# Kernel optimization log

Hardware: AMD Instinct MI355X
Metric: run time of the kernel (lower is better)

The kernel has to match this reference:

```python
import jax, jax.numpy as jnp
import numpy as np

IGNORE = 255
KA = 10.0
ITERS = 10
BETA = 0.8


def _l2(x, axis):
    # F.normalize(p=2): divide by max(norm, eps)
    return x / jnp.maximum(jnp.linalg.norm(x, axis=axis, keepdims=True), 1e-12)


def setup_inputs() -> dict:
    key = jax.random.key(0)
    k1, k2, k3, k4 = jax.random.split(key, 4)
    B, K, P, C = 8, 19, 16384, 256
    return {
        "logit": jax.random.normal(k1, (B, K, P), jnp.float32),
        "target": jax.random.randint(k2, (B, P), 0, K, jnp.int32),
        "feat": jax.random.normal(k3, (B, C, P), jnp.float32),
        "epoch": 60,
        "prototypes_dataset": _l2(jax.random.normal(k4, (C, K), jnp.float32), 0),
    }


def reference(logit, target, feat, epoch, prototypes_dataset):
    B, K, P = logit.shape
    C = feat.shape[1]
    dt = feat.dtype

    # scatter-sum per-class prototypes over all (b, p) positions; ignore bucket = K
    index = jnp.where(target == IGNORE, K, target).reshape(-1)            # [B*P]
    feat_flat = jnp.swapaxes(feat, 1, 2).reshape(B * P, C)                # [B*P, C]
    proto = jax.ops.segment_sum(feat_flat, index, num_segments=K + 1)    # [K+1, C]
    counts = jax.ops.segment_sum(jnp.ones_like(index), index, num_segments=K + 1)
    prototypes_sum = proto[:K].T                                          # [C, K]
    counts_batch = counts[:K]                                             # [K]

    # epoch is a static python int; epoch >= start_epoch(51) -> full vMF branch
    feat_norm = _l2(feat, 1)                                              # [B, C, P]
    u_init = _l2(prototypes_sum / (counts_batch.astype(dt) + 1e-6), 0)    # [C, K]
    mask0 = counts_batch == 0
    u = _l2(jnp.where(mask0[None, :], prototypes_dataset, u_init), 0)     # 'part' init
    a = jnp.full((1, 1, K), 1.0 / K, dt)

    dis = jnp.einsum('bcp,ck->bpk', feat_norm, u)                         # [B, P, K]
    e = a * jnp.exp(KA * dis)
    p = e / jnp.sum(e, -1, keepdims=True)
    for _ in range(ITERS):
        # 'avmf': second assignment in torch overwrites -> mean over batch, [1, P, K]
        a = jnp.mean(p, 0, keepdims=True)
        # 'uvmf': new prototypes from soft assignments
        u = _l2(jnp.mean(jnp.einsum('bcp,bpk->bck', feat_norm, p), 0), 0)
        dis = jnp.einsum('bcp,ck->bpk', feat_norm, u)
        e = a * jnp.exp(KA * dis)
        p = e / jnp.sum(e, -1, keepdims=True)

    # vMF_hard_loss computed in torch but 'hard' not in loss_type -> not added
    vmf_loss = jnp.mean(-p * (jnp.log(a + 1e-6) + KA * dis)) / float(np.log(K))
    consist_loss = jnp.mean(-jnp.swapaxes(p, 1, 2) * jax.nn.log_softmax(logit, axis=1))

    # contrast: off-diagonal prototype similarity over classes present in batch
    m = (~mask0).astype(dt)
    gram = u_init.T @ u_init                                              # [K, K]
    Kn = jnp.sum(m)
    contrast_loss = (jnp.sum(gram * (m[:, None] * m[None, :])) - Kn) / (Kn * (Kn - 1))

    # 'tce': truncated CE, clamp per-pixel loss at -log(beta)
    logp = jax.nn.log_softmax(logit, axis=1)                              # [B, K, P]
    safe_t = jnp.where(target == IGNORE, 0, target)
    ce = -jnp.take_along_axis(logp, safe_t[:, None, :], axis=1)[:, 0, :]  # [B, P]
    valid = (target != IGNORE).astype(dt)
    loss = jnp.sum(jnp.maximum(ce, -float(np.log(BETA))) * valid) / (jnp.sum(valid) + 1e-6)

    loss = loss + vmf_loss + contrast_loss + consist_loss
    return (loss, jax.lax.stop_gradient(prototypes_sum), jax.lax.stop_gradient(counts_batch))
```

## Files before the change

kernel.cpp:

```cpp
#include <hip/hip_runtime.h>
#include <hip/hip_bf16.h>
#include <math.h>

#define BB 8
#define KK 19
#define PP 16384
#define CC 256
#define NN (BB*PP)
#define KA_C 10.0f
#define IGNORE_L 255
#define CETHR 0.22314355131420976f
#define AQ 524288

#define OFF_FEATN   0
#define OFF_FEATNT  16777216
#define OFF_PROTO   33554432
#define OFF_COUNTS  (OFF_PROTO+4864)
#define OFF_SCAL    (OFF_COUNTS+32)
#define OFF_UINIT   (OFF_SCAL+16)
#define OFF_U       (OFF_UINIT+4864)
#define OFF_UBF     (OFF_U+4864)
#define OFF_A       (OFF_UBF+4224)
#define OFF_UPART   (OFF_A+8*AQ)
#define OFF_R1      (OFF_UPART+4980736)
#define OFF_NORM    (OFF_R1+77824)

typedef __attribute__((ext_vector_type(8))) short short8v;
typedef __attribute__((ext_vector_type(4))) float f32x4;

static __device__ __forceinline__ float bflo(unsigned int v){
    union{unsigned int i; float f;} x; x.i = v << 16; return x.f;
}
static __device__ __forceinline__ unsigned short f2bf(float f){
    union{float f; unsigned int i;} x; x.f = f;
    unsigned int r = (x.i + 0x7fffu + ((x.i >> 16) & 1u)) >> 16;
    return (unsigned short)r;
}
static __device__ __forceinline__ float rowsum16(float v){
    v += __shfl_xor(v,1); v += __shfl_xor(v,2);
    v += __shfl_xor(v,4); v += __shfl_xor(v,8);
    return v;
}

__global__ __launch_bounds__(256) void counts_kernel(const int* __restrict__ target,
                                                     float* __restrict__ ws) {
    __shared__ int cnt[KK];
    if (threadIdx.x < KK) cnt[threadIdx.x]=0;
    __syncthreads();
    for (int i = blockIdx.x*256 + threadIdx.x; i < NN; i += gridDim.x*256) {
        int t = target[i];
        if (t >= 0 && t < KK) atomicAdd(&cnt[t], 1);
    }
    __syncthreads();
    if (threadIdx.x < KK) atomicAdd(&ws[OFF_COUNTS + threadIdx.x], (float)cnt[threadIdx.x]);
}

__global__ __launch_bounds__(256) void ssct_kernel(const float* __restrict__ feat,
                                                   unsigned short* __restrict__ featn,
                                                   unsigned short* __restrict__ featn_T,
                                                   float* __restrict__ normf) {
    __shared__ float part[4][64];
    __shared__ float rn_lds[64];
    __shared__ unsigned short tTus[64][270];
    int blk = blockIdx.x;
    int b = blk >> 8;
    int px0 = (blk & 255) * 64;
    int tid = threadIdx.x;
    int l = tid & 63, w = tid >> 6;
    const float* fb = feat + (size_t)b*CC*PP;
    int c0 = w*64;
    float ss = 0.f;
    for (int cc=0; cc<64; cc++) {
        float v = fb[(size_t)(c0+cc)*PP + px0 + l];
        ss = fmaf(v, v, ss);
    }
    part[w][l] = ss;
    __syncthreads();
    if (tid < 64) {
        float s = part[0][tid]+part[1][tid]+part[2][tid]+part[3][tid];
        float nrm = fmaxf(sqrtf(s), 1e-12f);
        normf[(size_t)b*PP + px0 + tid] = nrm;
        rn_lds[tid] = 1.0f/nrm;
    }
    __syncthreads();
    float r = rn_lds[l];
    unsigned short* ob  = featn + (size_t)b*CC*PP + px0;
    for (int cc=0; cc<64; cc++) {
        int c = c0 + cc;
        float v = fb[(size_t)c*PP + px0 + l];
        unsigned short us = f2bf(v * r);
        ob[(size_t)c*PP + l] = us;
        tTus[l][c] = us;
    }
    __syncthreads();
    unsigned short* obT = featn_T + ((size_t)b*PP + px0)*CC;
    for (int j=0; j<32; j++) {
        int flat = j*256 + tid;
        int px = flat >> 7, cu = flat & 127;
        unsigned int v = *(const unsigned int*)&tTus[px][cu*2];
        *(unsigned int*)&obT[(size_t)px*CC + cu*2] = v;
    }
}

__global__ __launch_bounds__(256) void proto_mfma_kernel(const unsigned short* __restrict__ featn,
                                                         const int* __restrict__ target,
                                                         const float* __restrict__ normf,
                                                         float* __restrict__ upart) {
    __shared__ int tgt_lds[4][64];
    __shared__ unsigned short nrm_lds[4][64];
    int tid = threadIdx.x;
    int blk = blockIdx.x;
    int pxtile = blk & 255;
    int bgrp = blk >> 8;
    {
        int bi = tid >> 6, j = tid & 63;
        int bb = bgrp*4 + bi;
        tgt_lds[bi][j] = target[(size_t)bb*PP + pxtile*64 + j];
        nrm_lds[bi][j] = f2bf(normf[(size_t)bb*PP + pxtile*64 + j]);
    }
    __syncthreads();
    int lane = tid & 63, wid = tid >> 6;
    int g = lane >> 4, lc = lane & 15;

    f32x4 upacc[4][2];
#pragma unroll
    for (int m=0;m<4;m++)
#pragma unroll
        for (int n=0;n<2;n++) upacc[m][n] = (f32x4){0.f,0.f,0.f,0.f};

    for (int bi=0; bi<4; bi++) {
        int bb = bgrp*4 + bi;
        union { unsigned int u[4]; short8v s; } bfr[2][2];
#pragma unroll
        for (int ks=0; ks<2; ks++) {
            int pxo = ks*32 + g*8;
#pragma unroll
            for (int j2=0;j2<4;j2++) {
                int p0i = pxo + 2*j2, p1i = pxo + 2*j2 + 1;
                int t0 = tgt_lds[bi][p0i], t1 = tgt_lds[bi][p1i];
                unsigned int n0 = nrm_lds[bi][p0i], n1 = nrm_lds[bi][p1i];
                int kk1 = lc + 16;
                bfr[ks][0].u[j2] = (t0==lc ? n0:0u) | ((t1==lc ? n1:0u)<<16);
                bfr[ks][1].u[j2] = (t0==kk1? n0:0u) | ((t1==kk1? n1:0u)<<16);
            }
        }
#pragma unroll
        for (int m=0;m<4;m++) {
            int c = wid*64 + m*16 + lc;
            const unsigned short* fr = featn + ((size_t)bb*CC + c)*PP + pxtile*64;
#pragma unroll
            for (int ks=0; ks<2; ks++) {
                int pxo = ks*32 + g*8;
                union { uint4 u4; short8v s; } af2;
                af2.u4 = *(const uint4*)&fr[pxo];
                upacc[m][0] = __builtin_amdgcn_mfma_f32_16x16x32_bf16(af2.s, bfr[ks][0].s, upacc[m][0], 0,0,0);
                upacc[m][1] = __builtin_amdgcn_mfma_f32_16x16x32_bf16(af2.s, bfr[ks][1].s, upacc[m][1], 0,0,0);
            }
        }
    }
#pragma unroll
    for (int m=0;m<4;m++) {
        int cb = wid*64 + m*16 + g*4;
#pragma unroll
        for (int n=0;n<2;n++) {
            int kk = lc + 16*n;
            if (kk < KK) {
#pragma unroll
                for (int r=0;r<4;r++)
                    upart[(size_t)blk*4864 + (size_t)(cb+r)*KK + kk] = upacc[m][n][r];
            }
        }
    }
}

__global__ __launch_bounds__(256) void setup_kernel(const float* __restrict__ pd,
                                                    float* __restrict__ ws) {
    int c = threadIdx.x;
    __shared__ float red[256];
    __shared__ float nrm[KK];
    __shared__ float lds_ui[256][KK];
    float cnts[KK], vi[KK];
#pragma unroll
    for (int k=0;k<KK;k++) cnts[k] = ws[OFF_COUNTS+k];
#pragma unroll
    for (int k=0;k<KK;k++) vi[k] = ws[OFF_PROTO + c*KK + k] / (cnts[k] + 1e-6f);
    for (int k=0;k<KK;k++) {
        red[c] = vi[k]*vi[k];
        __syncthreads();
        for (int s=128;s>0;s>>=1){ if (c<s) red[c]+=red[c+s]; __syncthreads(); }
        if (c==0) nrm[k] = fmaxf(sqrtf(red[0]), 1e-12f);
        __syncthreads();
    }
#pragma unroll
    for (int k=0;k<KK;k++) { vi[k] = vi[k]/nrm[k]; lds_ui[c][k] = vi[k]; ws[OFF_UINIT + c*KK + k] = vi[k]; }
    __syncthreads();
    float w0[KK];
#pragma unroll
    for (int k=0;k<KK;k++) w0[k] = (cnts[k]==0.f) ? pd[c*KK+k] : vi[k];
    for (int k=0;k<KK;k++) {
        red[c] = w0[k]*w0[k];
        __syncthreads();
        for (int s=128;s>0;s>>=1){ if (c<s) red[c]+=red[c+s]; __syncthreads(); }
        if (c==0) nrm[k] = fmaxf(sqrtf(red[0]), 1e-12f);
        __syncthreads();
    }
    unsigned short* ubf = (unsigned short*)(ws + OFF_UBF);
#pragma unroll
    for (int k=0;k<KK;k++) {
        float uv = w0[k] / nrm[k];
        ws[OFF_U + k*CC + c] = uv;
        ubf[k*264 + c] = f2bf(uv);
    }
    float m[KK]; float Kn=0.f;
#pragma unroll
    for (int k=0;k<KK;k++){ m[k] = (cnts[k]==0.f)?0.f:1.f; Kn += m[k]; }
    float csum = 0.f;
    for (int idx = c; idx < KK*KK; idx += 256) {
        int k1 = idx / KK, k2 = idx % KK;
        if (m[k1]!=0.f && m[k2]!=0.f) {
            float gg=0.f;
            for (int cc2=0; cc2<CC; cc2++) gg += lds_ui[cc2][k1]*lds_ui[cc2][k2];
            csum += gg;
        }
    }
    red[c]=csum; __syncthreads();
    for (int s=128;s>0;s>>=1){ if (c<s) red[c]+=red[c+s]; __syncthreads(); }
    if (c==0) ws[OFF_SCAL+4] = (red[0] - Kn) / (Kn * (Kn - 1.f));
}

__global__ __launch_bounds__(256) void pu_kernel(const unsigned short* __restrict__ featn,
                                                 const unsigned short* __restrict__ featn_T,
                                                 const unsigned short* __restrict__ ubf,
                                                 const float* __restrict__ aRbase,
                                                 float* __restrict__ aWbase,
                                                 float* __restrict__ upart,
                                                 int uniform_a) {
    __shared__ __attribute__((aligned(16))) unsigned short u_lds[32*264];
    __shared__ __attribute__((aligned(16))) unsigned short p_lds[32*72];
    int tid = threadIdx.x;
    {
        const uint4* src = (const uint4*)ubf;
        uint4* dst = (uint4*)u_lds;
        for (int i=tid; i<1056; i+=256) dst[i] = src[i];
    }
    __syncthreads();
    int blk = blockIdx.x;
    int pxtile = blk & 255;
    int bgrp = blk >> 8;
    int lane = tid & 63, wid = tid >> 6;
    int g = lane >> 4, lc = lane & 15;
    int px_w = pxtile*64 + wid*16;

    float a0r[4], a1r[4];
    if (uniform_a) {
#pragma unroll
        for (int r=0;r<4;r++){ a0r[r]=1.0f/(float)KK; a1r[r]=1.0f/(float)KK; }
    } else {
        int k1 = (lc+16 > KK-1) ? (KK-1) : (lc+16);
#pragma unroll
        for (int r=0;r<4;r++) {
            int pxg = px_w + g*4 + r;
            float s0 = aRbase[0*AQ + (size_t)pxg*32 + lc] + aRbase[1*AQ + (size_t)pxg*32 + lc]
                     + aRbase[2*AQ + (size_t)pxg*32 + lc] + aRbase[3*AQ + (size_t)pxg*32 + lc];
            float s1 = aRbase[0*AQ + (size_t)pxg*32 + k1] + aRbase[1*AQ + (size_t)pxg*32 + k1]
                     + aRbase[2*AQ + (size_t)pxg*32 + k1] + aRbase[3*AQ + (size_t)pxg*32 + k1];
            a0r[r] = s0*0.125f;
            a1r[r] = s1*0.125f;
        }
    }

    f32x4 upacc[4][2];
#pragma unroll
    for (int m=0;m<4;m++)
#pragma unroll
        for (int n=0;n<2;n++) upacc[m][n] = (f32x4){0.f,0.f,0.f,0.f};
    float aacc[2][4];
#pragma unroll
    for (int n=0;n<2;n++)
#pragma unroll
        for (int r=0;r<4;r++) aacc[n][r]=0.f;

    for (int bi=0; bi<2; bi++) {
        int bb = bgrp*2 + bi;
        const unsigned short* fb = featn + (size_t)bb*CC*PP;
        const unsigned short* fTrow = featn_T + ((size_t)bb*PP + px_w + lc)*CC;
        f32x4 acc0 = (f32x4){0.f,0.f,0.f,0.f};
        f32x4 acc1 = (f32x4){0.f,0.f,0.f,0.f};
#pragma unroll
        for (int ks=0; ks<8; ks++) {
            int cbase = ks*32 + g*8;
            union { uint4 u4; short8v s; } af, bf0, bf1;
            af.u4  = *(const uint4*)&fTrow[cbase];
            bf0.u4 = *(const uint4*)&u_lds[(size_t)lc*264 + cbase];
            bf1.u4 = *(const uint4*)&u_lds[(size_t)(lc+16)*264 + cbase];
            acc0 = __builtin_amdgcn_mfma_f32_16x16x32_bf16(af.s, bf0.s, acc0, 0,0,0);
            acc1 = __builtin_amdgcn_mfma_f32_16x16x32_bf16(af.s, bf1.s, acc1, 0,0,0);
        }
#pragma unroll
        for (int r=0;r<4;r++) {
            float e0 = a0r[r] * __expf(KA_C * acc0[r]);
            float e1 = (lc+16 < KK) ? a1r[r] * __expf(KA_C * acc1[r]) : 0.f;
            float sv = rowsum16(e0 + e1);
            float inv = 1.0f/sv;
            float p0 = e0*inv, p1 = e1*inv;
            aacc[0][r] += p0; aacc[1][r] += p1;
            int pl = wid*16 + g*4 + r;
            p_lds[(size_t)lc*72 + pl]      = f2bf(p0);
            p_lds[(size_t)(lc+16)*72 + pl] = f2bf(p1);
        }
        __syncthreads();
#pragma unroll
        for (int m=0;m<4;m++) {
            int c = wid*64 + m*16 + lc;
            const unsigned short* fr = fb + (size_t)c*PP + pxtile*64;
#pragma unroll
            for (int ks=0; ks<2; ks++) {
                int pxo = ks*32 + g*8;
                union { uint4 u4; short8v s; } af2, bp0, bp1;
                af2.u4 = *(const uint4*)&fr[pxo];
                bp0.u4 = *(const uint4*)&p_lds[(size_t)lc*72 + pxo];
                bp1.u4 = *(const uint4*)&p_lds[(size_t)(lc+16)*72 + pxo];
                upacc[m][0] = __builtin_amdgcn_mfma_f32_16x16x32_bf16(af2.s, bp0.s, upacc[m][0], 0,0,0);
                upacc[m][1] = __builtin_amdgcn_mfma_f32_16x16x32_bf16(af2.s, bp1.s, upacc[m][1], 0,0,0);
            }
        }
        __syncthreads();
    }
#pragma unroll
    for (int m=0;m<4;m++) {
        int cb = wid*64 + m*16 + g*4;
#pragma unroll
        for (int n=0;n<2;n++) {
            int kk = lc + 16*n;
            if (kk < KK) {
#pragma unroll
                for (int r=0;r<4;r++)
                    upart[(size_t)blk*4864 + (size_t)(cb+r)*KK + kk] = upacc[m][n][r];
            }
        }
    }
    float* aOut = aWbase + (size_t)bgrp*AQ;
#pragma unroll
    for (int n=0;n<2;n++) {
        int kk = lc + 16*n;
        if (kk < KK) {
#pragma unroll
            for (int r=0;r<4;r++) {
                int pxg = px_w + g*4 + r;
                aOut[(size_t)pxg*32 + kk] = aacc[n][r];
            }
        }
    }
}

__global__ __launch_bounds__(256) void r1_kernel(const float* __restrict__ upart,
                                                 float* __restrict__ r1buf) {
    int blk = blockIdx.x;
    int echunk = blk % 19;
    int ichunk = blk / 19;
    int e = echunk*256 + threadIdx.x;
    float s = 0.f;
    int i0 = ichunk*64;
    for (int i=i0; i<i0+64; i++) s += upart[(size_t)i*4864 + e];
    r1buf[(size_t)ichunk*4864 + e] = s;
}

__global__ __launch_bounds__(256) void r2_kernel(const float* __restrict__ r1buf,
                                                 float* __restrict__ ws, int nbuf) {
    int k = blockIdx.x;
    int c = threadIdx.x;
    float s = 0.f;
    for (int i=0;i<nbuf;i++) s += r1buf[(size_t)i*4864 + c*KK + k];
    __shared__ float red[256];
    red[c] = s*s; __syncthreads();
    for (int q=128;q>0;q>>=1){ if (c<q) red[c]+=red[c+q]; __syncthreads(); }
    float nrm = fmaxf(sqrtf(red[0]), 1e-12f);
    float uv = s / nrm;
    ws[OFF_U + k*CC + c] = uv;
    ((unsigned short*)(ws + OFF_UBF))[k*264 + c] = f2bf(uv);
}

__global__ __launch_bounds__(256) void protored2_kernel(const float* __restrict__ r1buf,
                                                        float* __restrict__ ws, int nbuf) {
    int e = blockIdx.x*256 + threadIdx.x;
    float s = 0.f;
    for (int i=0;i<nbuf;i++) s += r1buf[(size_t)i*4864 + e];
    ws[OFF_PROTO + e] = s;
}

__global__ __launch_bounds__(256) void final_kernel(const unsigned short* __restrict__ featn,
                                                    const float* __restrict__ logit,
                                                    const int* __restrict__ target,
                                                    const float* __restrict__ ws_u,
                                                    const float* __restrict__ aFbase,
                                                    float* __restrict__ scal) {
    __shared__ float lu[4864];
    for (int i=threadIdx.x; i<4864; i+=256) lu[i] = ws_u[i];
    __syncthreads();
    int n = blockIdx.x*256 + threadIdx.x;
    int b = n >> 14;
    int pix = n & (PP-1);
    const unsigned short* fcol = featn + (size_t)b*CC*PP + pix;
    float dot[KK];
#pragma unroll
    for (int k=0;k<KK;k++) dot[k]=0.f;
    for (int c0=0; c0<CC; c0+=16) {
        float fv[16];
#pragma unroll
        for (int j=0;j<16;j++) {
            unsigned int u16 = fcol[(size_t)(c0+j)*PP];
            fv[j] = bflo(u16);
        }
#pragma unroll
        for (int k=0;k<KK;k++) {
            float d = dot[k];
#pragma unroll
            for (int j=0;j<16;j++) d = fmaf(fv[j], lu[k*CC+c0+j], d);
            dot[k]=d;
        }
    }
    float e[KK]; float den=0.f; float av[KK];
#pragma unroll
    for (int k=0;k<KK;k++) {
        av[k] = (aFbase[0*AQ + (size_t)pix*32 + k] + aFbase[1*AQ + (size_t)pix*32 + k]
               + aFbase[2*AQ + (size_t)pix*32 + k] + aFbase[3*AQ + (size_t)pix*32 + k])*0.125f;
        e[k] = av[k] * __expf(KA_C * dot[k]);
        den += e[k];
    }
    float inv = 1.0f/den;
    float vmf = 0.f;
#pragma unroll
    for (int k=0;k<KK;k++) {
        vmf += -(e[k]*inv) * (__logf(av[k] + 1e-6f) + KA_C * dot[k]);
    }
    float lg[KK]; float mx = -3.4e38f;
#pragma unroll
    for (int k=0;k<KK;k++) { lg[k] = logit[((size_t)b*KK + k)*PP + pix]; mx = fmaxf(mx, lg[k]); }
    float sme = 0.f;
#pragma unroll
    for (int k=0;k<KK;k++) sme += __expf(lg[k]-mx);
    float lse = mx + __logf(sme);
    float cons = 0.f;
#pragma unroll
    for (int k=0;k<KK;k++) cons += -(e[k]*inv) * (lg[k]-lse);
    int t = target[(size_t)b*PP + pix];
    float ce_n = 0.f, ce_d = 0.f;
    if (t != IGNORE_L) {
        float lt = 0.f;
#pragma unroll
        for (int k=0;k<KK;k++) lt = (t==k) ? lg[k] : lt;
        float ce = -(lt - lse);
        ce_n = fmaxf(ce, CETHR);
        ce_d = 1.f;
    }
    __shared__ float red[4][4];
    int lane = threadIdx.x & 63, w = threadIdx.x >> 6;
    float v0=vmf, v1=cons, v2=ce_n, v3=ce_d;
#pragma unroll
    for (int s=32;s>0;s>>=1) {
        v0 += __shfl_xor(v0, s); v1 += __shfl_xor(v1, s);
        v2 += __shfl_xor(v2, s); v3 += __shfl_xor(v3, s);
    }
    if (lane==0){ red[w][0]=v0; red[w][1]=v1; red[w][2]=v2; red[w][3]=v3; }
    __syncthreads();
    if (threadIdx.x==0) {
        atomicAdd(&scal[0], red[0][0]+red[1][0]+red[2][0]+red[3][0]);
        atomicAdd(&scal[1], red[0][1]+red[1][1]+red[2][1]+red[3][1]);
        atomicAdd(&scal[2], red[0][2]+red[1][2]+red[2][2]+red[3][2]);
        atomicAdd(&scal[3], red[0][3]+red[1][3]+red[2][3]+red[3][3]);
    }
}

__global__ __launch_bounds__(256) void finalize_kernel(const float* __restrict__ ws,
                                                       float* __restrict__ out) {
    if (blockIdx.x==0 && threadIdx.x==0) {
        float cnt_all = (float)BB*(float)PP*(float)KK;
        float vmf  = ws[OFF_SCAL+0] / cnt_all / logf((float)KK);
        float cons = ws[OFF_SCAL+1] / cnt_all;
        float ce   = ws[OFF_SCAL+2] / (ws[OFF_SCAL+3] + 1e-6f);
        float contrast = ws[OFF_SCAL+4];
        out[0] = ce + vmf + contrast + cons;
    }
    int i = blockIdx.x*256 + threadIdx.x;
    if (i < 4864) out[1+i] = ws[OFF_PROTO+i];
    if (blockIdx.x==0 && threadIdx.x < KK) out[1+4864+threadIdx.x] = ws[OFF_COUNTS+threadIdx.x];
}

extern "C" void kernel_launch(void* const* d_in, const int* in_sizes, int n_in,
                              void* d_out, int out_size, void* d_ws, size_t ws_size,
                              hipStream_t stream) {
    (void)in_sizes; (void)n_in; (void)out_size; (void)ws_size;
    const float* logit  = (const float*)d_in[0];
    const int*   target = (const int*)d_in[1];
    const float* feat   = (const float*)d_in[2];
    const float* pd     = (const float*)d_in[4];
    float* out = (float*)d_out;
    float* ws  = (float*)d_ws;

    unsigned short* featn   = (unsigned short*)ws;
    unsigned short* featn_T = (unsigned short*)(ws + OFF_FEATNT);
    unsigned short* ubf     = (unsigned short*)(ws + OFF_UBF);
    float* ubuf  = ws + OFF_U;
    float* upart = ws + OFF_UPART;
    float* r1buf = ws + OFF_R1;
    float* normf = ws + OFF_NORM;
    float* scal  = ws + OFF_SCAL;
    float* aSet[2] = { ws + OFF_A, ws + OFF_A + (size_t)4*AQ };

    hipMemsetAsync(ws + OFF_PROTO, 0, 4912*sizeof(float), stream);
    hipMemsetAsync(ws + OFF_UBF, 0, 4224*sizeof(float), stream);
    ssct_kernel<<<2048, 256, 0, stream>>>(feat, featn, featn_T, normf);
    counts_kernel<<<256, 256, 0, stream>>>(target, ws);
    proto_mfma_kernel<<<512, 256, 0, stream>>>(featn, target, normf, upart);
    r1_kernel<<<152, 256, 0, stream>>>(upart, r1buf);
    protored2_kernel<<<19, 256, 0, stream>>>(r1buf, ws, 8);
    setup_kernel<<<1, 256, 0, stream>>>(pd, ws);

    for (int t=0; t<10; t++) {
        if (t > 0) {
            r1_kernel<<<304, 256, 0, stream>>>(upart, r1buf);
            r2_kernel<<<KK, 256, 0, stream>>>(r1buf, ws, 16);
        }
        pu_kernel<<<1024, 256, 0, stream>>>(featn, featn_T, ubf,
                                            aSet[t&1], aSet[(t+1)&1],
                                            upart, (t==0)?1:0);
    }
    r1_kernel<<<304, 256, 0, stream>>>(upart, r1buf);
    r2_kernel<<<KK, 256, 0, stream>>>(r1buf, ws, 16);
    final_kernel<<<512, 256, 0, stream>>>(featn, logit, target, ubuf, aSet[0], scal);
    finalize_kernel<<<20, 256, 0, stream>>>(ws, out);
}
```

Before: 617.0 us.

## Compute final vMF loss pass with bf16 MFMA and cache feature loads in ssct

The final loss kernel's per-pixel scalar dot products against the 19 prototypes are replaced by bf16 MFMA tiles over the transposed normalized features. The per-class softmax, vMF, consistency and CE terms are then reduced with 16-lane shuffles. A new kernel transposes the logits into a padded pixel-major layout so each row can be read per lane. Separately, the normalization kernel keeps its 64 feature values in registers instead of reading them from global memory twice. The extra transpose pass and the higher register pressure may offset some of the savings.

Measured after the change: 594.8 us. -3.6%, faster.

```diff
diff --git a/kernel.cpp b/kernel.cpp
--- a/kernel.cpp
+++ b/kernel.cpp
@@ -24,6 +24,7 @@
 #define OFF_UPART   (OFF_A+8*AQ)
 #define OFF_R1      (OFF_UPART+4980736)
 #define OFF_NORM    (OFF_R1+77824)
+#define OFF_LOGT    (OFF_NORM+131072)
 
 typedef __attribute__((ext_vector_type(8))) short short8v;
 typedef __attribute__((ext_vector_type(4))) float f32x4;
@@ -39,6 +40,11 @@
 static __device__ __forceinline__ float rowsum16(float v){
     v += __shfl_xor(v,1); v += __shfl_xor(v,2);
     v += __shfl_xor(v,4); v += __shfl_xor(v,8);
+    return v;
+}
+static __device__ __forceinline__ float rowmax16(float v){
+    v = fmaxf(v, __shfl_xor(v,1)); v = fmaxf(v, __shfl_xor(v,2));
+    v = fmaxf(v, __shfl_xor(v,4)); v = fmaxf(v, __shfl_xor(v,8));
     return v;
 }
 
@@ -69,10 +75,12 @@
     int l = tid & 63, w = tid >> 6;
     const float* fb = feat + (size_t)b*CC*PP;
     int c0 = w*64;
+    float fv[64];
     float ss = 0.f;
+#pragma unroll
     for (int cc=0; cc<64; cc++) {
-        float v = fb[(size_t)(c0+cc)*PP + px0 + l];
-        ss = fmaf(v, v, ss);
+        fv[cc] = fb[(size_t)(c0+cc)*PP + px0 + l];
+        ss = fmaf(fv[cc], fv[cc], ss);
     }
     part[w][l] = ss;
     __syncthreads();
@@ -85,10 +93,10 @@
     __syncthreads();
     float r = rn_lds[l];
     unsigned short* ob  = featn + (size_t)b*CC*PP + px0;
+#pragma unroll
     for (int cc=0; cc<64; cc++) {
         int c = c0 + cc;
-        float v = fb[(size_t)c*PP + px0 + l];
-        unsigned short us = f2bf(v * r);
+        unsigned short us = f2bf(fv[cc] * r);
         ob[(size_t)c*PP + l] = us;
         tTus[l][c] = us;
     }
@@ -99,6 +107,24 @@
         int px = flat >> 7, cu = flat & 127;
         unsigned int v = *(const unsigned int*)&tTus[px][cu*2];
         *(unsigned int*)&obT[(size_t)px*CC + cu*2] = v;
+    }
+}
+
+__global__ __launch_bounds__(256) void logt_kernel(const float* __restrict__ logit,
+                                                   float* __restrict__ logt) {
+    __shared__ float t[256][21];
+    int blk = blockIdx.x;
+    int b = blk >> 6;
+    int px0 = (blk & 63) * 256;
+    int tid = threadIdx.x;
+    for (int k=0;k<KK;k++)
+        t[tid][k] = logit[((size_t)b*KK + k)*PP + px0 + tid];
+    __syncthreads();
+    float* dst = logt + ((size_t)b*PP + px0)*20;
+    for (int j=0; j<20; j++) {
+        int flat = j*256 + tid;
+        int px = flat / 20, k = flat % 20;
+        dst[flat] = (k<KK) ? t[px][k] : 0.f;
     }
 }
 
@@ -388,82 +414,96 @@
     ws[OFF_PROTO + e] = s;
 }
 
-__global__ __launch_bounds__(256) void final_kernel(const unsigned short* __restrict__ featn,
-                                                    const float* __restrict__ logit,
-                                                    const int* __restrict__ target,
-                                                    const float* __restrict__ ws_u,
-                                                    const float* __restrict__ aFbase,
-                                                    float* __restrict__ scal) {
-    __shared__ float lu[4864];
-    for (int i=threadIdx.x; i<4864; i+=256) lu[i] = ws_u[i];
-    __syncthreads();
-    int n = blockIdx.x*256 + threadIdx.x;
-    int b = n >> 14;
-    int pix = n & (PP-1);
-    const unsigned short* fcol = featn + (size_t)b*CC*PP + pix;
-    float dot[KK];
-#pragma unroll
-    for (int k=0;k<KK;k++) dot[k]=0.f;
-    for (int c0=0; c0<CC; c0+=16) {
-        float fv[16];
-#pragma unroll
-        for (int j=0;j<16;j++) {
-            unsigned int u16 = fcol[(size_t)(c0+j)*PP];
-            fv[j] = bflo(u16);
-        }
-#pragma unroll
-        for (int k=0;k<KK;k++) {
-            float d = dot[k];
-#pragma unroll
-            for (int j=0;j<16;j++) d = fmaf(fv[j], lu[k*CC+c0+j], d);
-            dot[k]=d;
-        }
-    }
-    float e[KK]; float den=0.f; float av[KK];
-#pragma unroll
-    for (int k=0;k<KK;k++) {
-        av[k] = (aFbase[0*AQ + (size_t)pix*32 + k] + aFbase[1*AQ + (size_t)pix*32 + k]
-               + aFbase[2*AQ + (size_t)pix*32 + k] + aFbase[3*AQ + (size_t)pix*32 + k])*0.125f;
-        e[k] = av[k] * __expf(KA_C * dot[k]);
-        den += e[k];
-    }
-    float inv = 1.0f/den;
-    float vmf = 0.f;
-#pragma unroll
-    for (int k=0;k<KK;k++) {
-        vmf += -(e[k]*inv) * (__logf(av[k] + 1e-6f) + KA_C * dot[k]);
-    }
-    float lg[KK]; float mx = -3.4e38f;
-#pragma unroll
-    for (int k=0;k<KK;k++) { lg[k] = logit[((size_t)b*KK + k)*PP + pix]; mx = fmaxf(mx, lg[k]); }
-    float sme = 0.f;
-#pragma unroll
-    for (int k=0;k<KK;k++) sme += __expf(lg[k]-mx);
-    float lse = mx + __logf(sme);
-    float cons = 0.f;
-#pragma unroll
-    for (int k=0;k<KK;k++) cons += -(e[k]*inv) * (lg[k]-lse);
-    int t = target[(size_t)b*PP + pix];
-    float ce_n = 0.f, ce_d = 0.f;
-    if (t != IGNORE_L) {
-        float lt = 0.f;
-#pragma unroll
-        for (int k=0;k<KK;k++) lt = (t==k) ? lg[k] : lt;
-        float ce = -(lt - lse);
-        ce_n = fmaxf(ce, CETHR);
-        ce_d = 1.f;
+__global__ __launch_bounds__(256) void final_mfma_kernel(const unsigned short* __restrict__ featn_T,
+                                                         const float* __restrict__ logt,
+                                                         const int* __restrict__ target,
+                                                         const unsigned short* __restrict__ ubf,
+                                                         const float* __restrict__ aFbase,
+                                                         float* __restrict__ scal) {
+    __shared__ __attribute__((aligned(16))) unsigned short u_lds[32*264];
+    int tid = threadIdx.x;
+    {
+        const uint4* src = (const uint4*)ubf;
+        uint4* dst = (uint4*)u_lds;
+        for (int i=tid; i<1056; i+=256) dst[i] = src[i];
+    }
+    __syncthreads();
+    int blk = blockIdx.x;
+    int pxtile = blk & 255;
+    int bgrp = blk >> 8;
+    int lane = tid & 63, wid = tid >> 6;
+    int g = lane >> 4, lc = lane & 15;
+    int px_w = pxtile*64 + wid*16;
+    bool valid1 = (lc+16) < KK;
+
+    float v_vmf=0.f, v_cons=0.f, v_ce=0.f, v_cnt=0.f;
+
+    for (int bi=0; bi<4; bi++) {
+        int bb = bgrp*4 + bi;
+        const unsigned short* fTrow = featn_T + ((size_t)bb*PP + px_w + lc)*CC;
+        f32x4 acc0 = (f32x4){0.f,0.f,0.f,0.f};
+        f32x4 acc1 = (f32x4){0.f,0.f,0.f,0.f};
+#pragma unroll
+        for (int ks=0; ks<8; ks++) {
+            int cbase = ks*32 + g*8;
+            union { uint4 u4; short8v s; } af, bf0, bf1;
+            af.u4  = *(const uint4*)&fTrow[cbase];
+            bf0.u4 = *(const uint4*)&u_lds[(size_t)lc*264 + cbase];
+            bf1.u4 = *(const uint4*)&u_lds[(size_t)(lc+16)*264 + cbase];
+            acc0 = __builtin_amdgcn_mfma_f32_16x16x32_bf16(af.s, bf0.s, acc0, 0,0,0);
+            acc1 = __builtin_amdgcn_mfma_f32_16x16x32_bf16(af.s, bf1.s, acc1, 0,0,0);
+        }
+#pragma unroll
+        for (int r=0;r<4;r++) {
+            int pxg = px_w + g*4 + r;
+            float d0 = acc0[r], d1 = acc1[r];
+            float av0 = (aFbase[0*AQ + (size_t)pxg*32 + lc] + aFbase[1*AQ + (size_t)pxg*32 + lc]
+                       + aFbase[2*AQ + (size_t)pxg*32 + lc] + aFbase[3*AQ + (size_t)pxg*32 + lc])*0.125f;
+            float av1 = 0.f;
+            if (valid1) {
+                int k1 = lc+16;
+                av1 = (aFbase[0*AQ + (size_t)pxg*32 + k1] + aFbase[1*AQ + (size_t)pxg*32 + k1]
+                     + aFbase[2*AQ + (size_t)pxg*32 + k1] + aFbase[3*AQ + (size_t)pxg*32 + k1])*0.125f;
+            }
+            float e0 = av0 * __expf(KA_C * d0);
+            float e1 = valid1 ? av1 * __expf(KA_C * d1) : 0.f;
+            float den = rowsum16(e0 + e1);
+            float inv = 1.0f/den;
+            float p0 = e0*inv, p1 = e1*inv;
+            float vt = -p0*(__logf(av0+1e-6f) + KA_C*d0);
+            if (valid1) vt += -p1*(__logf(av1+1e-6f) + KA_C*d1);
+            float vt_row = rowsum16(vt);
+            const float* lrow = logt + ((size_t)bb*PP + pxg)*20;
+            float lg0 = lrow[lc];
+            float lg1 = valid1 ? lrow[lc+16] : -3.4e38f;
+            float mx = rowmax16(fmaxf(lg0, lg1));
+            float sme = __expf(lg0-mx) + (valid1 ? __expf(lg1-mx) : 0.f);
+            sme = rowsum16(sme);
+            float lse = mx + __logf(sme);
+            float ct = -p0*(lg0-lse);
+            if (valid1) ct += -p1*(lg1-lse);
+            float ct_row = rowsum16(ct);
+            int t = target[(size_t)bb*PP + pxg];
+            float ltt = (lc==t ? lg0 : 0.f) + ((valid1 && lc+16==t) ? lg1 : 0.f);
+            float lt = rowsum16(ltt);
+            if (lc==0) {
+                v_vmf += vt_row;
+                v_cons += ct_row;
+                if (t != IGNORE_L) { v_ce += fmaxf(lse - lt, CETHR); v_cnt += 1.f; }
+            }
+        }
     }
     __shared__ float red[4][4];
-    int lane = threadIdx.x & 63, w = threadIdx.x >> 6;
-    float v0=vmf, v1=cons, v2=ce_n, v3=ce_d;
+    int w = tid >> 6;
+    float v0=v_vmf, v1=v_cons, v2=v_ce, v3=v_cnt;
 #pragma unroll
     for (int s=32;s>0;s>>=1) {
         v0 += __shfl_xor(v0, s); v1 += __shfl_xor(v1, s);
         v2 += __shfl_xor(v2, s); v3 += __shfl_xor(v3, s);
     }
-    if (lane==0){ red[w][0]=v0; red[w][1]=v1; red[w][2]=v2; red[w][3]=v3; }
-    __syncthreads();
-    if (threadIdx.x==0) {
+    if ((tid&63)==0){ red[w][0]=v0; red[w][1]=v1; red[w][2]=v2; red[w][3]=v3; }
+    __syncthreads();
+    if (tid==0) {
         atomicAdd(&scal[0], red[0][0]+red[1][0]+red[2][0]+red[3][0]);
         atomicAdd(&scal[1], red[0][1]+red[1][1]+red[2][1]+red[3][1]);
         atomicAdd(&scal[2], red[0][2]+red[1][2]+red[2][2]+red[3][2]);
@@ -500,10 +540,10 @@
     unsigned short* featn   = (unsigned short*)ws;
     unsigned short* featn_T = (unsigned short*)(ws + OFF_FEATNT);
     unsigned short* ubf     = (unsigned short*)(ws + OFF_UBF);
-    float* ubuf  = ws + OFF_U;
     float* upart = ws + OFF_UPART;
     float* r1buf = ws + OFF_R1;
     float* normf = ws + OFF_NORM;
+    float* logt  = ws + OFF_LOGT;
     float* scal  = ws + OFF_SCAL;
     float* aSet[2] = { ws + OFF_A, ws + OFF_A + (size_t)4*AQ };
 
@@ -511,6 +551,7 @@
     hipMemsetAsync(ws + OFF_UBF, 0, 4224*sizeof(float), stream);
     ssct_kernel<<<2048, 256, 0, stream>>>(feat, featn, featn_T, normf);
     counts_kernel<<<256, 256, 0, stream>>>(target, ws);
+    logt_kernel<<<512, 256, 0, stream>>>(logit, logt);
     proto_mfma_kernel<<<512, 256, 0, stream>>>(featn, target, normf, upart);
     r1_kernel<<<152, 256, 0, stream>>>(upart, r1buf);
     protored2_kernel<<<19, 256, 0, stream>>>(r1buf, ws, 8);
@@ -527,6 +568,6 @@
     }
     r1_kernel<<<304, 256, 0, stream>>>(upart, r1buf);
     r2_kernel<<<KK, 256, 0, stream>>>(r1buf, ws, 16);
-    final_kernel<<<512, 256, 0, stream>>>(featn, logit, target, ubuf, aSet[0], scal);
+    final_mfma_kernel<<<512, 256, 0, stream>>>(featn_T, logt, target, ubf, aSet[0], scal);
     finalize_kernel<<<20, 256, 0, stream>>>(ws, out);
 }
```
